# Performance work log

Measured on AMD Instinct MI355X. Metric: run time of the kernel, lower is better.

The kernel has to match this reference:

```python
import jax, jax.numpy as jnp
import numpy as np

TEMPERATURE = 0.07
NEG_INF_FILL = -1e9  # matches torch fill_diagonal_(-1000000000.0)


def setup_inputs() -> dict:
    key = jax.random.key(0)
    feats = jax.random.normal(key, (6144, 768), dtype=jnp.float32)
    return {"feats": feats}


def reference(feats):
    # L2-normalize rows (torch F.normalize uses eps=1e-12 clamp on the norm)
    norm = jnp.maximum(jnp.linalg.norm(feats, axis=1, keepdims=True), 1e-12)
    f = feats / norm
    N = f.shape[0]
    sim = jnp.matmul(f, f.T) / TEMPERATURE            # [N, N]
    eye = jnp.eye(N, dtype=bool)
    sim = jnp.where(eye, NEG_INF_FILL, sim)           # fill diagonal
    labels = jnp.arange(N) // 3                       # 3 views per slice
    pos = (labels[:, None] == labels[None, :]) & ~eye  # positives, self excluded
    # masked logsumexp over positives via weights b (grad-safe masking)
    numerator = jax.scipy.special.logsumexp(sim, axis=1, b=pos.astype(sim.dtype))
    denominator = jax.scipy.special.logsumexp(sim, axis=1)
    loss = jnp.sum(-(numerator - denominator)) / N
    return loss
```

## Files before the change

kernel.cpp:

```cpp
#include <hip/hip_runtime.h>

#define NN 6144
#define DD 768
#define NB 48
#define NTILES 1176
#define INV_T 14.285714285714286f
#define CMAX  14.285714285714286f

typedef int i32x4 __attribute__((ext_vector_type(4)));
typedef int i32x8 __attribute__((ext_vector_type(8)));
typedef float f32x4_t __attribute__((ext_vector_type(4)));

__device__ __forceinline__ void load_lds16(const void* g, void* l) {
    __builtin_amdgcn_global_load_lds((__attribute__((address_space(1))) void*)g,
                                     (__attribute__((address_space(3))) void*)l,
                                     16, 0, 0);
}

__global__ void norm_kernel(const float* __restrict__ feats,
                            unsigned int* __restrict__ fb8,
                            float* __restrict__ den_num) {
    const int wid = threadIdx.x >> 6;
    const int lane = threadIdx.x & 63;
    const int row = blockIdx.x * 4 + wid;

    if (threadIdx.x < 8) den_num[blockIdx.x * 8 + threadIdx.x] = 0.0f;

    const float4* src = (const float4*)(feats + (size_t)row * DD);
    float4 v[3];
    float ss = 0.0f;
#pragma unroll
    for (int i = 0; i < 3; ++i) {
        v[i] = src[lane + i * 64];
        ss += v[i].x * v[i].x + v[i].y * v[i].y + v[i].z * v[i].z + v[i].w * v[i].w;
    }
#pragma unroll
    for (int m = 32; m >= 1; m >>= 1) ss += __shfl_xor(ss, m);
    const float sc = 1.0f / fmaxf(sqrtf(ss), 1e-12f);

#pragma unroll
    for (int i = 0; i < 3; ++i) {
        unsigned int w = 0;
        w = __builtin_amdgcn_cvt_pk_fp8_f32(v[i].x * sc, v[i].y * sc, w, 0);
        w = __builtin_amdgcn_cvt_pk_fp8_f32(v[i].z * sc, v[i].w * sc, w, 1);
        fb8[(size_t)row * 192 + lane + i * 64] = w;
    }
}

__global__ __launch_bounds__(256, 2) void gemm_expsum_kernel(
        const unsigned char* __restrict__ fb8,
        float* __restrict__ den_sum, float* __restrict__ num_sum) {
    __shared__ __align__(16) char sA[128 * 128];
    __shared__ __align__(16) char sB[128 * 128];

    int rem = blockIdx.x;
    int bi = 0, rowlen = NB;
    while (rem >= rowlen) { rem -= rowlen; rowlen--; bi++; }
    const int bj = bi + rem;
    const bool isdiag = (bi == bj);
    const bool neardiag = (bj - bi) <= 1;
    const int i0 = bi * 128;
    const int j0 = bj * 128;

    const int t = threadIdx.x;
    const int lane = t & 63;
    const int wid = t >> 6;
    const int wm = wid >> 1;
    const int wn = wid & 1;

    const int srow = t >> 3;
    const int scb = ((t & 7) ^ (srow & 7)) * 16;
    const unsigned char* gA = fb8 + (size_t)(i0 + srow) * DD + scb;
    const unsigned char* gB = fb8 + (size_t)(j0 + srow) * DD + scb;
    char* ldsA = sA + wid * 1024;
    char* ldsB = sB + wid * 1024;

    f32x4_t acc[4][4];
    const f32x4_t zz = {0.0f, 0.0f, 0.0f, 0.0f};
#pragma unroll
    for (int mi = 0; mi < 4; ++mi)
#pragma unroll
        for (int ni = 0; ni < 4; ++ni) acc[mi][ni] = zz;

    const int q = lane >> 4;
    const int mrow = lane & 15;
    const int x7 = lane & 7;
    const int c0 = ((q << 1) ^ x7) << 4;
    const int c1 = (((q << 1) | 1) ^ x7) << 4;

#pragma unroll 1
    for (int kb = 0; kb < 6; ++kb) {
        const int k0 = kb * 128;
#pragma unroll
        for (int i = 0; i < 4; ++i) {
            load_lds16(gA + (size_t)(i * 32) * DD + k0, ldsA + i * 4096);
            load_lds16(gB + (size_t)(i * 32) * DD + k0, ldsB + i * 4096);
        }
        __syncthreads();

        i32x8 af[4];
#pragma unroll
        for (int mi = 0; mi < 4; ++mi) {
            const char* p = sA + (wm * 64 + mi * 16 + mrow) * 128;
            i32x4 lo = *(const i32x4*)(p + c0);
            i32x4 hi = *(const i32x4*)(p + c1);
            af[mi] = __builtin_shufflevector(lo, hi, 0, 1, 2, 3, 4, 5, 6, 7);
        }
#pragma unroll
        for (int ni = 0; ni < 4; ++ni) {
            const char* p = sB + (wn * 64 + ni * 16 + mrow) * 128;
            i32x4 lo = *(const i32x4*)(p + c0);
            i32x4 hi = *(const i32x4*)(p + c1);
            i32x8 bf = __builtin_shufflevector(lo, hi, 0, 1, 2, 3, 4, 5, 6, 7);
#pragma unroll
            for (int mi = 0; mi < 4; ++mi)
                acc[mi][ni] = __builtin_amdgcn_mfma_scale_f32_16x16x128_f8f6f4(
                    af[mi], bf, acc[mi][ni], 0, 0,
                    0, 0x7F7F7F7F, 0, 0x7F7F7F7F);
        }
        __syncthreads();
    }

    const int colb = j0 + wn * 64 + mrow;
    const int rowb = i0 + wm * 64 + (q << 2);
    float cs[4] = {0.f, 0.f, 0.f, 0.f};
    float csn[4] = {0.f, 0.f, 0.f, 0.f};
#pragma unroll
    for (int mi = 0; mi < 4; ++mi) {
        float rsv[4] = {0.f, 0.f, 0.f, 0.f};
        float rsn[4] = {0.f, 0.f, 0.f, 0.f};
#pragma unroll
        for (int ni = 0; ni < 4; ++ni) {
            const int col = colb + ni * 16;
#pragma unroll
            for (int r = 0; r < 4; ++r) {
                const int row = rowb + mi * 16 + r;
                const float v = acc[mi][ni][r] * INV_T;
                float e = __expf(v - CMAX);
                if (isdiag && row == col) e = 0.0f;
                rsv[r] += e;
                cs[ni] += e;
                if (neardiag && (row / 3 == col / 3) && row != col) {
                    rsn[r] += e;
                    csn[ni] += e;
                }
            }
        }
#pragma unroll
        for (int r = 0; r < 4; ++r) {
            float v = rsv[r];
            v += __shfl_xor(v, 8);
            v += __shfl_xor(v, 4);
            v += __shfl_xor(v, 2);
            v += __shfl_xor(v, 1);
            if (mrow == 0) atomicAdd(&den_sum[rowb + mi * 16 + r], v);
        }
        if (neardiag) {
#pragma unroll
            for (int r = 0; r < 4; ++r) {
                float v = rsn[r];
                v += __shfl_xor(v, 8);
                v += __shfl_xor(v, 4);
                v += __shfl_xor(v, 2);
                v += __shfl_xor(v, 1);
                if (mrow == 0) atomicAdd(&num_sum[rowb + mi * 16 + r], v);
            }
        }
    }
    if (!isdiag) {
#pragma unroll
        for (int ni = 0; ni < 4; ++ni) {
            float v = cs[ni];
            v += __shfl_xor(v, 16);
            v += __shfl_xor(v, 32);
            if (q == 0) atomicAdd(&den_sum[colb + ni * 16], v);
        }
        if (neardiag) {
#pragma unroll
            for (int ni = 0; ni < 4; ++ni) {
                float v = csn[ni];
                v += __shfl_xor(v, 16);
                v += __shfl_xor(v, 32);
                if (q == 0) atomicAdd(&num_sum[colb + ni * 16], v);
            }
        }
    }
}

__global__ void finalize_kernel(const float* __restrict__ den_sum,
                                const float* __restrict__ num_sum,
                                float* __restrict__ out) {
    float local = 0.0f;
    for (int i = threadIdx.x; i < NN; i += 256) {
        local += logf(den_sum[i]) - logf(num_sum[i]);
    }
#pragma unroll
    for (int m = 32; m >= 1; m >>= 1) local += __shfl_xor(local, m);
    __shared__ float ws[4];
    if ((threadIdx.x & 63) == 0) ws[threadIdx.x >> 6] = local;
    __syncthreads();
    if (threadIdx.x == 0) out[0] = (ws[0] + ws[1] + ws[2] + ws[3]) / (float)NN;
}

extern "C" void kernel_launch(void* const* d_in, const int* in_sizes, int n_in,
                              void* d_out, int out_size, void* d_ws, size_t ws_size,
                              hipStream_t stream) {
    const float* feats = (const float*)d_in[0];
    float* out = (float*)d_out;

    char* ws = (char*)d_ws;
    unsigned int* fb8 = (unsigned int*)ws;
    float* den_num    = (float*)(ws + 4718592);
    float* den_sum    = den_num;
    float* num_sum    = den_num + NN;

    norm_kernel<<<NN / 4, 256, 0, stream>>>(feats, fb8, den_num);
    gemm_expsum_kernel<<<NTILES, 256, 0, stream>>>((const unsigned char*)fb8,
                                                   den_sum, num_sum);
    finalize_kernel<<<1, 256, 0, stream>>>(den_sum, num_sum, out);
}
```

Baseline: 110.6 us.

## Load MFMA operands directly from global memory, dropping LDS staging

Removes the shared-memory tiles and barriers from the FP8 GEMM. Each wave now reads its 32-byte fragments straight from global memory (mostly L2) into registers. This eliminates the LDS round trip and both __syncthreads per k-step. In exchange, operands are no longer shared across waves, so global and L2 traffic roughly doubles, and loads are no longer prefetched while the barrier waits.

```diff
diff --git a/kernel.cpp b/kernel.cpp
--- a/kernel.cpp
+++ b/kernel.cpp
@@ -7,15 +7,8 @@
 #define INV_T 14.285714285714286f
 #define CMAX  14.285714285714286f
 
-typedef int i32x4 __attribute__((ext_vector_type(4)));
 typedef int i32x8 __attribute__((ext_vector_type(8)));
 typedef float f32x4_t __attribute__((ext_vector_type(4)));
-
-__device__ __forceinline__ void load_lds16(const void* g, void* l) {
-    __builtin_amdgcn_global_load_lds((__attribute__((address_space(1))) void*)g,
-                                     (__attribute__((address_space(3))) void*)l,
-                                     16, 0, 0);
-}
 
 __global__ void norm_kernel(const float* __restrict__ feats,
                             unsigned int* __restrict__ fb8,
@@ -50,9 +43,6 @@
 __global__ __launch_bounds__(256, 2) void gemm_expsum_kernel(
         const unsigned char* __restrict__ fb8,
         float* __restrict__ den_sum, float* __restrict__ num_sum) {
-    __shared__ __align__(16) char sA[128 * 128];
-    __shared__ __align__(16) char sB[128 * 128];
-
     int rem = blockIdx.x;
     int bi = 0, rowlen = NB;
     while (rem >= rowlen) { rem -= rowlen; rowlen--; bi++; }
@@ -68,12 +58,11 @@
     const int wm = wid >> 1;
     const int wn = wid & 1;
 
-    const int srow = t >> 3;
-    const int scb = ((t & 7) ^ (srow & 7)) * 16;
-    const unsigned char* gA = fb8 + (size_t)(i0 + srow) * DD + scb;
-    const unsigned char* gB = fb8 + (size_t)(j0 + srow) * DD + scb;
-    char* ldsA = sA + wid * 1024;
-    char* ldsB = sB + wid * 1024;
+    const int q = lane >> 4;
+    const int mrow = lane & 15;
+
+    const unsigned char* pA = fb8 + (size_t)(i0 + wm * 64 + mrow) * DD + q * 32;
+    const unsigned char* pB = fb8 + (size_t)(j0 + wn * 64 + mrow) * DD + q * 32;
 
     f32x4_t acc[4][4];
     const f32x4_t zz = {0.0f, 0.0f, 0.0f, 0.0f};
@@ -82,43 +71,22 @@
 #pragma unroll
         for (int ni = 0; ni < 4; ++ni) acc[mi][ni] = zz;
 
-    const int q = lane >> 4;
-    const int mrow = lane & 15;
-    const int x7 = lane & 7;
-    const int c0 = ((q << 1) ^ x7) << 4;
-    const int c1 = (((q << 1) | 1) ^ x7) << 4;
-
 #pragma unroll 1
     for (int kb = 0; kb < 6; ++kb) {
         const int k0 = kb * 128;
-#pragma unroll
-        for (int i = 0; i < 4; ++i) {
-            load_lds16(gA + (size_t)(i * 32) * DD + k0, ldsA + i * 4096);
-            load_lds16(gB + (size_t)(i * 32) * DD + k0, ldsB + i * 4096);
-        }
-        __syncthreads();
-
         i32x8 af[4];
 #pragma unroll
-        for (int mi = 0; mi < 4; ++mi) {
-            const char* p = sA + (wm * 64 + mi * 16 + mrow) * 128;
-            i32x4 lo = *(const i32x4*)(p + c0);
-            i32x4 hi = *(const i32x4*)(p + c1);
-            af[mi] = __builtin_shufflevector(lo, hi, 0, 1, 2, 3, 4, 5, 6, 7);
-        }
+        for (int mi = 0; mi < 4; ++mi)
+            af[mi] = *(const i32x8*)(pA + (size_t)mi * 16 * DD + k0);
 #pragma unroll
         for (int ni = 0; ni < 4; ++ni) {
-            const char* p = sB + (wn * 64 + ni * 16 + mrow) * 128;
-            i32x4 lo = *(const i32x4*)(p + c0);
-            i32x4 hi = *(const i32x4*)(p + c1);
-            i32x8 bf = __builtin_shufflevector(lo, hi, 0, 1, 2, 3, 4, 5, 6, 7);
+            const i32x8 bf = *(const i32x8*)(pB + (size_t)ni * 16 * DD + k0);
 #pragma unroll
             for (int mi = 0; mi < 4; ++mi)
                 acc[mi][ni] = __builtin_amdgcn_mfma_scale_f32_16x16x128_f8f6f4(
                     af[mi], bf, acc[mi][ni], 0, 0,
                     0, 0x7F7F7F7F, 0, 0x7F7F7F7F);
         }
-        __syncthreads();
     }
 
     const int colb = j0 + wn * 64 + mrow;
```

Result: slower. 148.9 us (+34.6%).
